# Optimization experiments

Hardware: AMD Instinct MI355X
Metric: run time of the kernel (lower is better)

Reference implementation:

```python
import jax, jax.numpy as jnp
import numpy as np

NUM_HEADS = 16


def _mhsa(x, Wq, Wk, Wv, Wo):
    B, S, D = x.shape
    H = NUM_HEADS
    dk = D // H
    # Linear applies weight [out, in]: y = x @ W.T
    Q = jnp.einsum('bsd,ed->bse', x, Wq).reshape(B, S, H, dk).transpose(0, 2, 1, 3)
    K = jnp.einsum('bsd,ed->bse', x, Wk).reshape(B, S, H, dk).transpose(0, 2, 1, 3)
    V = jnp.einsum('bsd,ed->bse', x, Wv).reshape(B, S, H, dk).transpose(0, 2, 1, 3)
    scores = jnp.einsum('bhqd,bhkd->bhqk', Q, K) / jnp.sqrt(jnp.asarray(dk, x.dtype))
    causal = jnp.tril(jnp.ones((S, S), dtype=bool))  # True = keep
    scores = jnp.where(causal, scores, jnp.asarray(-jnp.inf, x.dtype))
    attn = jax.nn.softmax(scores, axis=-1)
    out = jnp.einsum('bhqk,bhkd->bhqd', attn, V)  # [B,H,S,dk]
    out = out.transpose(0, 2, 1, 3).reshape(B, S, D)
    return jnp.einsum('bsd,ed->bse', out, Wo)


def setup_inputs() -> dict:
    key = jax.random.key(0)
    ks = jax.random.split(key, 5)
    B, S, D = 4, 2048, 1024
    std = 2.0 / (D + D) ** 0.5
    return {
        'x': jax.random.normal(ks[0], (B, S, D), dtype=jnp.float32),
        'Wq': jax.random.normal(ks[1], (D, D), dtype=jnp.float32) * std,
        'Wk': jax.random.normal(ks[2], (D, D), dtype=jnp.float32) * std,
        'Wv': jax.random.normal(ks[3], (D, D), dtype=jnp.float32) * std,
        'Wo': jax.random.normal(ks[4], (D, D), dtype=jnp.float32) * std,
    }


def reference(x, Wq, Wk, Wv, Wo):
    return _mhsa(x, Wq, Wk, Wv, Wo)
```

## Files before the change

kernel.cpp:

```cpp
#include <hip/hip_runtime.h>
#include <hip/hip_bf16.h>
#include <stdint.h>

typedef __attribute__((ext_vector_type(8))) short short8;
typedef __attribute__((ext_vector_type(4))) float f32x4;

static __device__ __forceinline__ void gload_lds16(const void* g, void* l) {
  __builtin_amdgcn_global_load_lds((const __attribute__((address_space(1))) void*)g,
                                   (__attribute__((address_space(3))) void*)l,
                                   16, 0, 0);
}

static __device__ __forceinline__ unsigned short f2bf(float f) {
  union { __hip_bfloat16 h; unsigned short s; } u;
  u.h = __float2bfloat16(f);
  return u.s;
}

__global__ void cast_f32_bf16(const float* __restrict__ src,
                              unsigned short* __restrict__ dst, int n4) {
  int i = blockIdx.x * 256 + threadIdx.x;
  if (i >= n4) return;
  float4 v = reinterpret_cast<const float4*>(src)[i];
  ushort4 o;
  o.x = f2bf(v.x); o.y = f2bf(v.y); o.z = f2bf(v.z); o.w = f2bf(v.w);
  reinterpret_cast<ushort4*>(dst)[i] = o;
}

template <typename OutT>
__global__ __launch_bounds__(256) void gemm_nt(const unsigned short* __restrict__ A,
                                               const unsigned short* __restrict__ B,
                                               OutT* __restrict__ C,
                                               int M, int N, int K) {
  __shared__ short sA[2][128 * 32];
  __shared__ short sB[2][128 * 32];
  const int t = threadIdx.x;
  const int w = t >> 6, l = t & 63, lg = l >> 4, lr = l & 15;
  const int wr = w >> 1, wc = w & 1;
  const int brow = blockIdx.y << 7, bcol = blockIdx.x << 7;

  f32x4 acc[4][4] = {};

  auto stage = [&](int buf, int kt) {
#pragma unroll
    for (int r = 0; r < 2; ++r) {
      const int byteoff = t * 16 + r * 4096;
      const int row = byteoff >> 6, inrow = byteoff & 63;
      gload_lds16((const char*)A + ((size_t)(brow + row) * K + kt) * 2 + inrow,
                  (char*)sA[buf] + byteoff);
      gload_lds16((const char*)B + ((size_t)(bcol + row) * K + kt) * 2 + inrow,
                  (char*)sB[buf] + byteoff);
    }
  };

  const int nkt = K >> 5;
  stage(0, 0);
  __syncthreads();
  int cur = 0;

  for (int kti = 0; kti < nkt; ++kti) {
    if (kti + 1 < nkt) stage(cur ^ 1, (kti + 1) << 5);

    short8 af[4], bfr[4];
#pragma unroll
    for (int m = 0; m < 4; ++m)
      af[m] = *reinterpret_cast<const short8*>(sA[cur] + (wr * 64 + m * 16 + lr) * 32 + lg * 8);
#pragma unroll
    for (int n = 0; n < 4; ++n)
      bfr[n] = *reinterpret_cast<const short8*>(sB[cur] + (wc * 64 + n * 16 + lr) * 32 + lg * 8);
#pragma unroll
    for (int m = 0; m < 4; ++m)
#pragma unroll
      for (int n = 0; n < 4; ++n)
        acc[m][n] = __builtin_amdgcn_mfma_f32_16x16x32_bf16(af[m], bfr[n], acc[m][n], 0, 0, 0);

    __syncthreads();
    cur ^= 1;
  }

#pragma unroll
  for (int m = 0; m < 4; ++m) {
#pragma unroll
    for (int n = 0; n < 4; ++n) {
#pragma unroll
      for (int j = 0; j < 4; ++j) {
        const int rr = brow + wr * 64 + m * 16 + lg * 4 + j;
        const int cc = bcol + wc * 64 + n * 16 + lr;
        if constexpr (sizeof(OutT) == 2) {
          C[(size_t)rr * N + cc] = (OutT)f2bf(acc[m][n][j]);
        } else {
          C[(size_t)rr * N + cc] = acc[m][n][j];
        }
      }
    }
  }
}

__global__ __launch_bounds__(256) void attn_kernel(const unsigned short* __restrict__ Qg,
                                                   const unsigned short* __restrict__ Kg,
                                                   const unsigned short* __restrict__ Vtg,
                                                   unsigned short* __restrict__ AO) {
  const int S = 2048, D = 1024, SN = 8192;
  const int i = blockIdx.x;
  const int lid = (i & 7) * 128 + (i >> 3);
  const int qp = lid & 15;
  const int bh = lid >> 4;
  const int b = bh >> 4, h = bh & 15;
  const int t = threadIdx.x;
  const int w = t >> 6, l = t & 63, lg = l >> 4, lr = l & 15;

  __shared__ short sK[2][64 * 64];
  __shared__ short sV[2][64 * 64];
  __shared__ short sP[4 * 16 * 64];

  int sboff[2], slin[2], srow[2];
#pragma unroll
  for (int r = 0; r < 2; ++r) {
    sboff[r] = t * 16 + r * 4096;
    srow[r] = sboff[r] >> 7;
    slin[r] = (sboff[r] & 127) ^ ((srow[r] & 7) << 4);
  }
  const char* Kbase = (const char*)Kg + ((size_t)(b * S) * D + h * 64) * 2;
  const char* Vbase = (const char*)Vtg + ((size_t)(h * 64) * SN + (size_t)b * S) * 2;

  auto stage = [&](int buf, int kvt) {
    const size_t kv0 = (size_t)kvt * 64;
#pragma unroll
    for (int r = 0; r < 2; ++r) {
      gload_lds16(Kbase + (kv0 + srow[r]) * 2048 + slin[r], (char*)sK[buf] + sboff[r]);
      gload_lds16(Vbase + (size_t)srow[r] * 16384 + kv0 * 2 + slin[r],
                  (char*)sV[buf] + sboff[r]);
    }
  };

  const float SCL = 0.125f * 1.44269504089f;
  int cur = 0;
  stage(0, 0);

#pragma unroll 1
  for (int half = 0; half < 2; ++half) {
    const int qt = half ? (31 - qp) : qp;
    const int nkv = qt + 1;

    short8 qf[2];
    {
      const unsigned short* qbase =
          Qg + (size_t)(b * S + qt * 64 + w * 16 + lr) * D + h * 64;
      qf[0] = *reinterpret_cast<const short8*>(qbase + lg * 8);
      qf[1] = *reinterpret_cast<const short8*>(qbase + 32 + lg * 8);
    }

    f32x4 o[4] = {};
    float m = -INFINITY, lsum = 0.f;

    __syncthreads();

    for (int kvt = 0; kvt < nkv; ++kvt) {
      if (kvt + 1 < nkv) stage(cur ^ 1, kvt + 1);

      const char* sKc = (const char*)sK[cur];
      const char* sVc = (const char*)sV[cur];

      f32x4 sc[4] = {};
#pragma unroll
      for (int n = 0; n < 4; ++n) {
#pragma unroll
        for (int kk = 0; kk < 2; ++kk) {
          const int row = n * 16 + lr;
          const short8 kf = *reinterpret_cast<const short8*>(
              sKc + (row << 7) + ((kk * 64 + lg * 16) ^ ((row & 7) << 4)));
          sc[n] = __builtin_amdgcn_mfma_f32_16x16x32_bf16(kf, qf[kk], sc[n], 0, 0, 0);
        }
      }

      float p[4][4];
      const bool diag = (kvt == qt);
      const int ql = w * 16 + lr;
#pragma unroll
      for (int n = 0; n < 4; ++n) {
#pragma unroll
        for (int r = 0; r < 4; ++r) {
          float v = sc[n][r] * SCL;
          if (diag && (n * 16 + lg * 4 + r) > ql) v = -INFINITY;
          p[n][r] = v;
        }
      }

      float mx = p[0][0];
#pragma unroll
      for (int n = 0; n < 4; ++n)
#pragma unroll
        for (int r = 0; r < 4; ++r) mx = fmaxf(mx, p[n][r]);
      mx = fmaxf(mx, __shfl_xor(mx, 16));
      mx = fmaxf(mx, __shfl_xor(mx, 32));
      const float mnew = fmaxf(m, mx);
      const float alpha = __builtin_amdgcn_exp2f(m - mnew);
      m = mnew;

      float s = 0.f;
#pragma unroll
      for (int n = 0; n < 4; ++n) {
#pragma unroll
        for (int r = 0; r < 4; ++r) {
          const float e = __builtin_amdgcn_exp2f(p[n][r] - mnew);
          p[n][r] = e;
          s += e;
        }
      }
      s += __shfl_xor(s, 16);
      s += __shfl_xor(s, 32);
      lsum = lsum * alpha + s;
#pragma unroll
      for (int dn = 0; dn < 4; ++dn) o[dn] *= alpha;

#pragma unroll
      for (int n = 0; n < 4; ++n) {
        ushort4 pk;
        pk.x = f2bf(p[n][0]); pk.y = f2bf(p[n][1]);
        pk.z = f2bf(p[n][2]); pk.w = f2bf(p[n][3]);
        *reinterpret_cast<ushort4*>(
            (char*)sP + (w << 11) + (lr << 7) + ((n * 32 + lg * 8) ^ ((lr & 7) << 4))) = pk;
      }

#pragma unroll
      for (int kk = 0; kk < 2; ++kk) {
        const short8 pa = *reinterpret_cast<const short8*>(
            (const char*)sP + (w << 11) + (lr << 7) +
            ((kk * 64 + lg * 16) ^ ((lr & 7) << 4)));
#pragma unroll
        for (int dn = 0; dn < 4; ++dn) {
          const int vrow = dn * 16 + lr;
          const short8 vb = *reinterpret_cast<const short8*>(
              sVc + (vrow << 7) + ((kk * 64 + lg * 16) ^ ((vrow & 7) << 4)));
          o[dn] = __builtin_amdgcn_mfma_f32_16x16x32_bf16(vb, pa, o[dn], 0, 0, 0);
        }
      }

      __syncthreads();
      cur ^= 1;
    }

    if (half == 0) stage(cur, 0);

    const float inv = 1.f / lsum;
    unsigned short* orow = AO + (size_t)(b * S + qt * 64 + w * 16 + lr) * D + h * 64;
#pragma unroll
    for (int dn = 0; dn < 4; ++dn) {
      ushort4 ov;
      ov.x = f2bf(o[dn][0] * inv); ov.y = f2bf(o[dn][1] * inv);
      ov.z = f2bf(o[dn][2] * inv); ov.w = f2bf(o[dn][3] * inv);
      *reinterpret_cast<ushort4*>(orow + dn * 16 + lg * 4) = ov;
    }
  }
}

extern "C" void kernel_launch(void* const* d_in, const int* in_sizes, int n_in,
                              void* d_out, int out_size, void* d_ws, size_t ws_size,
                              hipStream_t stream) {
  const float* x  = (const float*)d_in[0];
  const float* Wq = (const float*)d_in[1];
  const float* Wk = (const float*)d_in[2];
  const float* Wv = (const float*)d_in[3];
  const float* Wo = (const float*)d_in[4];
  float* out = (float*)d_out;

  char* ws = (char*)d_ws;
  unsigned short* xb  = (unsigned short*)(ws);
  unsigned short* Wqb = (unsigned short*)(ws + 16777216);
  unsigned short* Wkb = (unsigned short*)(ws + 18874368);
  unsigned short* Wvb = (unsigned short*)(ws + 20971520);
  unsigned short* Wob = (unsigned short*)(ws + 23068672);
  unsigned short* Qb  = (unsigned short*)(ws + 25165824);
  unsigned short* Kb  = (unsigned short*)(ws + 41943040);
  unsigned short* Vt  = (unsigned short*)(ws + 58720256);
  unsigned short* AO  = (unsigned short*)(ws + 75497472);

  cast_f32_bf16<<<8192, 256, 0, stream>>>(x,  xb,  2097152);
  cast_f32_bf16<<<1024, 256, 0, stream>>>(Wq, Wqb, 262144);
  cast_f32_bf16<<<1024, 256, 0, stream>>>(Wk, Wkb, 262144);
  cast_f32_bf16<<<1024, 256, 0, stream>>>(Wv, Wvb, 262144);
  cast_f32_bf16<<<1024, 256, 0, stream>>>(Wo, Wob, 262144);

  const dim3 blk(256);
  gemm_nt<unsigned short><<<dim3(8, 64), blk, 0, stream>>>(xb, Wqb, Qb, 8192, 1024, 1024);
  gemm_nt<unsigned short><<<dim3(8, 64), blk, 0, stream>>>(xb, Wkb, Kb, 8192, 1024, 1024);
  gemm_nt<unsigned short><<<dim3(64, 8), blk, 0, stream>>>(Wvb, xb, Vt, 1024, 8192, 1024);

  attn_kernel<<<dim3(1024), blk, 0, stream>>>(Qb, Kb, Vt, AO);

  gemm_nt<float><<<dim3(8, 64), blk, 0, stream>>>(AO, Wob, out, 8192, 1024, 1024);
}
```

Measured before the change: 288.7 us.

## Merge cast and QKV GEMM launches, add lazy softmax rescale and MFMA priority

The five cast kernels become one launch, and the three QKV projection GEMMs become one 1536-block launch with an XCD-aware block remap. The output GEMM also gets a block swizzle. The attention kernel now skips the online-softmax rescale unless some lane's max rises by more than 8 (log2 units), and raises wave priority around the MFMA sections. Together these cut launch overhead and tail effects, improve L2 locality, and remove exp and multiply work from the inner loop. The lazy rescale lets exponentials grow up to 2^8 before renormalising, which relies on fp32 range.

```diff
diff --git a/kernel.cpp b/kernel.cpp
--- a/kernel.cpp
+++ b/kernel.cpp
@@ -17,27 +17,43 @@
   return u.s;
 }
 
-__global__ void cast_f32_bf16(const float* __restrict__ src,
-                              unsigned short* __restrict__ dst, int n4) {
-  int i = blockIdx.x * 256 + threadIdx.x;
-  if (i >= n4) return;
-  float4 v = reinterpret_cast<const float4*>(src)[i];
+__global__ void cast_all(const float* __restrict__ x, const float* __restrict__ Wq,
+                         const float* __restrict__ Wk, const float* __restrict__ Wv,
+                         const float* __restrict__ Wo,
+                         unsigned short* __restrict__ xb, unsigned short* __restrict__ Wqb,
+                         unsigned short* __restrict__ Wkb, unsigned short* __restrict__ Wvb,
+                         unsigned short* __restrict__ Wob) {
+  const int i = blockIdx.x * 256 + threadIdx.x;
+  const float* src;
+  unsigned short* dst;
+  int off;
+  if (i < 2097152) {
+    src = x; dst = xb; off = i;
+  } else {
+    const int j = i - 2097152;
+    const int wsel = j >> 18;
+    off = j & 262143;
+    src = wsel == 0 ? Wq : wsel == 1 ? Wk : wsel == 2 ? Wv : Wo;
+    dst = wsel == 0 ? Wqb : wsel == 1 ? Wkb : wsel == 2 ? Wvb : Wob;
+  }
+  float4 v = reinterpret_cast<const float4*>(src)[off];
   ushort4 o;
   o.x = f2bf(v.x); o.y = f2bf(v.y); o.z = f2bf(v.z); o.w = f2bf(v.w);
-  reinterpret_cast<ushort4*>(dst)[i] = o;
+  reinterpret_cast<ushort4*>(dst)[off] = o;
 }
 
 template <typename OutT>
-__global__ __launch_bounds__(256) void gemm_nt(const unsigned short* __restrict__ A,
-                                               const unsigned short* __restrict__ B,
-                                               OutT* __restrict__ C,
-                                               int M, int N, int K) {
-  __shared__ short sA[2][128 * 32];
-  __shared__ short sB[2][128 * 32];
+static __device__ __forceinline__ void gemm_tile(const unsigned short* __restrict__ A,
+                                                 const unsigned short* __restrict__ B,
+                                                 OutT* __restrict__ C,
+                                                 int brow, int bcol, int ldc,
+                                                 short* sA0, short* sA1,
+                                                 short* sB0, short* sB1) {
   const int t = threadIdx.x;
   const int w = t >> 6, l = t & 63, lg = l >> 4, lr = l & 15;
   const int wr = w >> 1, wc = w & 1;
-  const int brow = blockIdx.y << 7, bcol = blockIdx.x << 7;
+  short* sAb[2] = {sA0, sA1};
+  short* sBb[2] = {sB0, sB1};
 
   f32x4 acc[4][4] = {};
 
@@ -46,28 +62,27 @@
     for (int r = 0; r < 2; ++r) {
       const int byteoff = t * 16 + r * 4096;
       const int row = byteoff >> 6, inrow = byteoff & 63;
-      gload_lds16((const char*)A + ((size_t)(brow + row) * K + kt) * 2 + inrow,
-                  (char*)sA[buf] + byteoff);
-      gload_lds16((const char*)B + ((size_t)(bcol + row) * K + kt) * 2 + inrow,
-                  (char*)sB[buf] + byteoff);
+      gload_lds16((const char*)A + ((size_t)(brow + row) * 1024 + kt) * 2 + inrow,
+                  (char*)sAb[buf] + byteoff);
+      gload_lds16((const char*)B + ((size_t)(bcol + row) * 1024 + kt) * 2 + inrow,
+                  (char*)sBb[buf] + byteoff);
     }
   };
 
-  const int nkt = K >> 5;
   stage(0, 0);
   __syncthreads();
   int cur = 0;
 
-  for (int kti = 0; kti < nkt; ++kti) {
-    if (kti + 1 < nkt) stage(cur ^ 1, (kti + 1) << 5);
+  for (int kti = 0; kti < 32; ++kti) {
+    if (kti + 1 < 32) stage(cur ^ 1, (kti + 1) << 5);
 
     short8 af[4], bfr[4];
 #pragma unroll
     for (int m = 0; m < 4; ++m)
-      af[m] = *reinterpret_cast<const short8*>(sA[cur] + (wr * 64 + m * 16 + lr) * 32 + lg * 8);
+      af[m] = *reinterpret_cast<const short8*>(sAb[cur] + (wr * 64 + m * 16 + lr) * 32 + lg * 8);
 #pragma unroll
     for (int n = 0; n < 4; ++n)
-      bfr[n] = *reinterpret_cast<const short8*>(sB[cur] + (wc * 64 + n * 16 + lr) * 32 + lg * 8);
+      bfr[n] = *reinterpret_cast<const short8*>(sBb[cur] + (wc * 64 + n * 16 + lr) * 32 + lg * 8);
 #pragma unroll
     for (int m = 0; m < 4; ++m)
 #pragma unroll
@@ -87,13 +102,50 @@
         const int rr = brow + wr * 64 + m * 16 + lg * 4 + j;
         const int cc = bcol + wc * 64 + n * 16 + lr;
         if constexpr (sizeof(OutT) == 2) {
-          C[(size_t)rr * N + cc] = (OutT)f2bf(acc[m][n][j]);
+          C[(size_t)rr * ldc + cc] = (OutT)f2bf(acc[m][n][j]);
         } else {
-          C[(size_t)rr * N + cc] = acc[m][n][j];
-        }
-      }
-    }
-  }
+          C[(size_t)rr * ldc + cc] = acc[m][n][j];
+        }
+      }
+    }
+  }
+}
+
+__global__ __launch_bounds__(256) void gemm_qkv(const unsigned short* __restrict__ xb,
+                                                const unsigned short* __restrict__ Wqb,
+                                                const unsigned short* __restrict__ Wkb,
+                                                const unsigned short* __restrict__ Wvb,
+                                                unsigned short* __restrict__ Qb,
+                                                unsigned short* __restrict__ Kb,
+                                                unsigned short* __restrict__ Vt) {
+  __shared__ short sA[2][4096];
+  __shared__ short sB[2][4096];
+  const int i = blockIdx.x;
+  const int lid = (i & 7) * 192 + (i >> 3);
+  const int z = lid >> 9, r = lid & 511;
+
+  const unsigned short *A, *B;
+  unsigned short* C;
+  int brow, bcol, ldc;
+  if (z == 2) {
+    A = Wvb; B = xb; C = Vt;
+    brow = (r & 7) << 7; bcol = (r >> 3) << 7; ldc = 8192;
+  } else {
+    A = xb; B = z ? Wkb : Wqb; C = z ? Kb : Qb;
+    brow = (r >> 3) << 7; bcol = (r & 7) << 7; ldc = 1024;
+  }
+  gemm_tile<unsigned short>(A, B, C, brow, bcol, ldc, sA[0], sA[1], sB[0], sB[1]);
+}
+
+__global__ __launch_bounds__(256) void gemm_out(const unsigned short* __restrict__ AO,
+                                                const unsigned short* __restrict__ Wob,
+                                                float* __restrict__ out) {
+  __shared__ short sA[2][4096];
+  __shared__ short sB[2][4096];
+  const int i = blockIdx.x;
+  const int lid = (i & 7) * 64 + (i >> 3);
+  gemm_tile<float>(AO, Wob, out, (lid >> 3) << 7, (lid & 7) << 7, 1024,
+                   sA[0], sA[1], sB[0], sB[1]);
 }
 
 __global__ __launch_bounds__(256) void attn_kernel(const unsigned short* __restrict__ Qg,
@@ -162,6 +214,7 @@
       const char* sVc = (const char*)sV[cur];
 
       f32x4 sc[4] = {};
+      __builtin_amdgcn_s_setprio(1);
 #pragma unroll
       for (int n = 0; n < 4; ++n) {
 #pragma unroll
@@ -172,6 +225,7 @@
           sc[n] = __builtin_amdgcn_mfma_f32_16x16x32_bf16(kf, qf[kk], sc[n], 0, 0, 0);
         }
       }
+      __builtin_amdgcn_s_setprio(0);
 
       float p[4][4];
       const bool diag = (kvt == qt);
@@ -193,25 +247,28 @@
         for (int r = 0; r < 4; ++r) mx = fmaxf(mx, p[n][r]);
       mx = fmaxf(mx, __shfl_xor(mx, 16));
       mx = fmaxf(mx, __shfl_xor(mx, 32));
-      const float mnew = fmaxf(m, mx);
-      const float alpha = __builtin_amdgcn_exp2f(m - mnew);
-      m = mnew;
+      if (!__all(mx <= m + 8.0f)) {
+        const float mnew = fmaxf(m, mx);
+        const float alpha = __builtin_amdgcn_exp2f(m - mnew);
+        m = mnew;
+        lsum *= alpha;
+#pragma unroll
+        for (int dn = 0; dn < 4; ++dn) o[dn] *= alpha;
+      }
 
       float s = 0.f;
 #pragma unroll
       for (int n = 0; n < 4; ++n) {
 #pragma unroll
         for (int r = 0; r < 4; ++r) {
-          const float e = __builtin_amdgcn_exp2f(p[n][r] - mnew);
+          const float e = __builtin_amdgcn_exp2f(p[n][r] - m);
           p[n][r] = e;
           s += e;
         }
       }
       s += __shfl_xor(s, 16);
       s += __shfl_xor(s, 32);
-      lsum = lsum * alpha + s;
-#pragma unroll
-      for (int dn = 0; dn < 4; ++dn) o[dn] *= alpha;
+      lsum += s;
 
 #pragma unroll
       for (int n = 0; n < 4; ++n) {
@@ -222,6 +279,7 @@
             (char*)sP + (w << 11) + (lr << 7) + ((n * 32 + lg * 8) ^ ((lr & 7) << 4))) = pk;
       }
 
+      __builtin_amdgcn_s_setprio(1);
 #pragma unroll
       for (int kk = 0; kk < 2; ++kk) {
         const short8 pa = *reinterpret_cast<const short8*>(
@@ -235,6 +293,7 @@
           o[dn] = __builtin_amdgcn_mfma_f32_16x16x32_bf16(vb, pa, o[dn], 0, 0, 0);
         }
       }
+      __builtin_amdgcn_s_setprio(0);
 
       __syncthreads();
       cur ^= 1;
@@ -275,18 +334,8 @@
   unsigned short* Vt  = (unsigned short*)(ws + 58720256);
   unsigned short* AO  = (unsigned short*)(ws + 75497472);
 
-  cast_f32_bf16<<<8192, 256, 0, stream>>>(x,  xb,  2097152);
-  cast_f32_bf16<<<1024, 256, 0, stream>>>(Wq, Wqb, 262144);
-  cast_f32_bf16<<<1024, 256, 0, stream>>>(Wk, Wkb, 262144);
-  cast_f32_bf16<<<1024, 256, 0, stream>>>(Wv, Wvb, 262144);
-  cast_f32_bf16<<<1024, 256, 0, stream>>>(Wo, Wob, 262144);
-
-  const dim3 blk(256);
-  gemm_nt<unsigned short><<<dim3(8, 64), blk, 0, stream>>>(xb, Wqb, Qb, 8192, 1024, 1024);
-  gemm_nt<unsigned short><<<dim3(8, 64), blk, 0, stream>>>(xb, Wkb, Kb, 8192, 1024, 1024);
-  gemm_nt<unsigned short><<<dim3(64, 8), blk, 0, stream>>>(Wvb, xb, Vt, 1024, 8192, 1024);
-
-  attn_kernel<<<dim3(1024), blk, 0, stream>>>(Qb, Kb, Vt, AO);
-
-  gemm_nt<float><<<dim3(8, 64), blk, 0, stream>>>(AO, Wob, out, 8192, 1024, 1024);
-}
+  cast_all<<<12288, 256, 0, stream>>>(x, Wq, Wk, Wv, Wo, xb, Wqb, Wkb, Wvb, Wob);
+  gemm_qkv<<<1536, 256, 0, stream>>>(xb, Wqb, Wkb, Wvb, Qb, Kb, Vt);
+  attn_kernel<<<1024, 256, 0, stream>>>(Qb, Kb, Vt, AO);
+  gemm_out<<<512, 256, 0, stream>>>(AO, Wob, out);
+}
```

After: 286.1 us. About the same (-0.9%).
